# Optimization experiments

Hardware: AMD Instinct MI355X
Metric: run time of the kernel (lower is better)

Reference implementation:

```python
import jax, jax.numpy as jnp
import numpy as np

B, T, D, H, L, V, CTX = 4, 2048, 256, 8, 12, 256, 2048
HD = D // H


def _ln(x, w, b, eps=1e-5):
    m = x.mean(-1, keepdims=True)
    v = ((x - m) ** 2).mean(-1, keepdims=True)
    return (x - m) * jax.lax.rsqrt(v + eps) * w + b


def setup_inputs() -> dict:
    key = jax.random.key(0)
    ks = jax.random.split(key, 16)
    s = 0.02
    inp = {
        "x": jax.random.randint(ks[0], (B, T), 0, V, dtype=jnp.int32),
        "tok_embed": jax.random.normal(ks[1], (V, D), jnp.float32) * s,
        "pos_embed": jax.random.normal(ks[2], (CTX, D), jnp.float32) * s,
        # stacked per-layer params (leading axis = layer)
        "ln1_w": jnp.ones((L, D), jnp.float32),
        "ln1_b": jnp.zeros((L, D), jnp.float32),
        "qkv_w": jax.random.normal(ks[3], (L, D, 3 * D), jnp.float32) * s,
        "qkv_b": jnp.zeros((L, 3 * D), jnp.float32),
        "out_w": jax.random.normal(ks[4], (L, D, D), jnp.float32) * s,
        "out_b": jnp.zeros((L, D), jnp.float32),
        "ln2_w": jnp.ones((L, D), jnp.float32),
        "ln2_b": jnp.zeros((L, D), jnp.float32),
        "fc1_w": jax.random.normal(ks[5], (L, D, 4 * D), jnp.float32) * s,
        "fc1_b": jnp.zeros((L, 4 * D), jnp.float32),
        "fc2_w": jax.random.normal(ks[6], (L, 4 * D, D), jnp.float32) * s,
        "fc2_b": jnp.zeros((L, D), jnp.float32),
        "lnf_w": jnp.ones((D,), jnp.float32),
        "lnf_b": jnp.zeros((D,), jnp.float32),
        "head_w": jax.random.normal(ks[7], (D, V), jnp.float32) * s,
        "head_b": jnp.zeros((V,), jnp.float32),
    }
    return inp


def _forward(x, tok_embed, pos_embed, ln1_w, ln1_b, qkv_w, qkv_b, out_w, out_b,
             ln2_w, ln2_b, fc1_w, fc1_b, fc2_w, fc2_b, lnf_w, lnf_b, head_w, head_b):
    Tcur = x.shape[1]
    h = tok_embed[x] + pos_embed[:Tcur][None, :, :]  # (B,T,D)
    causal = jnp.triu(jnp.ones((Tcur, Tcur), bool), k=1)  # True above diagonal
    scale = jnp.sqrt(jnp.asarray(HD, h.dtype))

    def step(h, p):
        (l1w, l1b, qw, qb, ow, ob, l2w, l2b, f1w, f1b, f2w, f2b) = p
        # attention
        z = _ln(h, l1w, l1b)
        qkv = z @ qw + qb  # (B,T,3D)
        qkv = qkv.reshape(h.shape[0], Tcur, 3, H, HD)
        q, k, v = qkv[:, :, 0], qkv[:, :, 1], qkv[:, :, 2]  # (B,T,H,HD)
        attn = jnp.einsum('bqhd,bkhd->bhqk', q, k) / scale
        attn = jnp.where(causal, -jnp.inf, attn)
        attn = jax.nn.softmax(attn, axis=-1)
        o = jnp.einsum('bhqk,bkhd->bqhd', attn, v).reshape(h.shape[0], Tcur, D)
        h = h + o @ ow + ob
        # MLP (torch nn.GELU default = exact erf gelu)
        z = _ln(h, l2w, l2b)
        z = jax.nn.gelu(z @ f1w + f1b, approximate=False)
        h = h + z @ f2w + f2b
        return h, None

    params = (ln1_w, ln1_b, qkv_w, qkv_b, out_w, out_b,
              ln2_w, ln2_b, fc1_w, fc1_b, fc2_w, fc2_b)
    h, _ = jax.lax.scan(step, h, params)
    h = _ln(h, lnf_w, lnf_b)
    return h @ head_w + head_b  # (B,T,V)


def reference(x, tok_embed, pos_embed, ln1_w, ln1_b, qkv_w, qkv_b, out_w, out_b,
              ln2_w, ln2_b, fc1_w, fc1_b, fc2_w, fc2_b, lnf_w, lnf_b, head_w, head_b):
    return _forward(x, tok_embed, pos_embed, ln1_w, ln1_b, qkv_w, qkv_b, out_w, out_b,
                    ln2_w, ln2_b, fc1_w, fc1_b, fc2_w, fc2_b, lnf_w, lnf_b, head_w, head_b)
```

## Files before the change

### kernel.cpp

```cpp
#include <hip/hip_runtime.h>
#include <cstdint>

#define TT 2048
#define DD 256
#define HH 8
#define LL 12

typedef __attribute__((ext_vector_type(8))) short s16x8;
typedef __attribute__((ext_vector_type(4))) float f32x4;

__device__ __forceinline__ unsigned short f2bf(float f) {
  union { float f; unsigned u; } v; v.f = f;
  return (unsigned short)((v.u + 0x7FFFu + ((v.u >> 16) & 1u)) >> 16);
}

__device__ __forceinline__ float geluf(float x) {
  return 0.5f * x * (1.0f + erff(x * 0.70710678118654752f));
}

__device__ __forceinline__ float fexp2(float x) {
  float r;
  asm("v_exp_f32 %0, %1" : "=v"(r) : "v"(x));
  return r;
}

__device__ __forceinline__ void gload16(const void* g, void* l) {
  __builtin_amdgcn_global_load_lds((const __attribute__((address_space(1))) unsigned int*)g,
                                   (__attribute__((address_space(3))) unsigned int*)l, 16, 0, 0);
}

__global__ __launch_bounds__(256) void k_embed(const int* __restrict__ x,
                                               const float* __restrict__ tok,
                                               const float* __restrict__ pos,
                                               float* __restrict__ h) {
  int i = blockIdx.x * 256 + threadIdx.x;
  int row = i >> 6, c = i & 63;
  int t = x[row];
  f32x4 tv = ((const f32x4*)(tok + (size_t)t * DD))[c];
  f32x4 pv = ((const f32x4*)(pos + (size_t)(row & (TT - 1)) * DD))[c];
  ((f32x4*)(h + (size_t)row * DD))[c] = tv + pv;
}

__global__ __launch_bounds__(256) void k_ln(const float* __restrict__ h,
                                            const float* __restrict__ wgt,
                                            const float* __restrict__ bia,
                                            unsigned short* __restrict__ z) {
  int row = blockIdx.x * 4 + (threadIdx.x >> 6);
  int lane = threadIdx.x & 63;
  f32x4 v = ((const f32x4*)(h + (size_t)row * DD))[lane];
  float s = v[0] + v[1] + v[2] + v[3];
#pragma unroll
  for (int m = 32; m; m >>= 1) s += __shfl_xor(s, m);
  float mean = s * (1.0f / DD);
  f32x4 d = v - mean;
  float s2 = d[0] * d[0] + d[1] * d[1] + d[2] * d[2] + d[3] * d[3];
#pragma unroll
  for (int m = 32; m; m >>= 1) s2 += __shfl_xor(s2, m);
  float inv = rsqrtf(s2 * (1.0f / DD) + 1e-5f);
  f32x4 wv = ((const f32x4*)wgt)[lane];
  f32x4 bv = ((const f32x4*)bia)[lane];
  union { unsigned short us[4]; unsigned long long u64; } ou;
#pragma unroll
  for (int e = 0; e < 4; ++e) ou.us[e] = f2bf(d[e] * inv * wv[e] + bv[e]);
  *(unsigned long long*)(z + (size_t)row * DD + lane * 4) = ou.u64;
}

__global__ __launch_bounds__(256) void k_cast_all(const float* __restrict__ qw, const float* __restrict__ ow,
                                                  const float* __restrict__ f1, const float* __restrict__ f2,
                                                  unsigned short* __restrict__ dst) {
  const int l = blockIdx.y;
  const int t0 = blockIdx.x * 256 + threadIdx.x;
  const int stride = gridDim.x * 256;
  const float* qwl = qw + (size_t)l * 196608;
  const float* owl = ow + (size_t)l * 65536;
  const float* f1l = f1 + (size_t)l * 262144;
  const float* f2l = f2 + (size_t)l * 262144;
  unsigned short* dq = dst + (size_t)l * 786432;
  unsigned short* dO = dq + 196608;
  unsigned short* d1 = dO + 65536;
  unsigned short* d2 = d1 + 262144;
  for (int i = t0; i < 196608; i += stride) { int k = i / 768, n = i % 768; dq[n * 256 + k] = f2bf(qwl[i]); }
  for (int i = t0; i < 65536; i += stride) { int k = i >> 8, n = i & 255; dO[n * 256 + k] = f2bf(owl[i]); }
  for (int i = t0; i < 262144; i += stride) { int k = i >> 10, n = i & 1023; d1[n * 256 + k] = f2bf(f1l[i]); }
  for (int i = t0; i < 262144; i += stride) { int k = i >> 8, n = i & 255; d2[n * 1024 + k] = f2bf(f2l[i]); }
}

__global__ __launch_bounds__(256) void k_cast_tr4(const float* __restrict__ qw, const float* __restrict__ ow,
                                                  const float* __restrict__ f1, const float* __restrict__ f2,
                                                  unsigned short* __restrict__ dq, unsigned short* __restrict__ dO,
                                                  unsigned short* __restrict__ d1, unsigned short* __restrict__ d2) {
  int t0 = blockIdx.x * 256 + threadIdx.x;
  int stride = gridDim.x * 256;
  for (int i = t0; i < 256 * 768; i += stride) { int k = i / 768, n = i % 768; dq[n * 256 + k] = f2bf(qw[i]); }
  for (int i = t0; i < 256 * 256; i += stride) { int k = i >> 8, n = i & 255; dO[n * 256 + k] = f2bf(ow[i]); }
  for (int i = t0; i < 256 * 1024; i += stride) { int k = i >> 10, n = i & 1023; d1[n * 256 + k] = f2bf(f1[i]); }
  for (int i = t0; i < 1024 * 256; i += stride) { int k = i >> 8, n = i & 255; d2[n * 1024 + k] = f2bf(f2[i]); }
}

__global__ __launch_bounds__(256) void k_cast_tr256(const float* __restrict__ src, unsigned short* __restrict__ dst) {
  int i = blockIdx.x * 256 + threadIdx.x;
  int k = i >> 8, n = i & 255;
  dst[n * 256 + k] = f2bf(src[i]);
}

template <int MODE, int MI>
__global__ __launch_bounds__(256) void k_gemm(const unsigned short* __restrict__ A,
                                              const unsigned short* __restrict__ BT,
                                              const float* __restrict__ bias,
                                              void* out, const float* resid,
                                              int M, int N, int K) {
  __shared__ __align__(16) unsigned short As[MI * 32 * 64];
  __shared__ __align__(16) unsigned short Bs[128 * 64];
  const int tid = threadIdx.x;
  const int lane = tid & 63, wv = tid >> 6;
  const int wr = wv >> 1, wc = wv & 1;
  const int l15 = lane & 15, g = lane >> 4;
  const int BM = MI * 32;
  const int tm = blockIdx.y, tn = blockIdx.x;
  f32x4 acc[MI][4] = {};
  const int nk = K >> 6;
  const unsigned short* Ag0 = A + (size_t)tm * BM * K;
  const unsigned short* Bg0 = BT + (size_t)tn * 128 * K;
  for (int kt = 0; kt < nk; ++kt) {
#pragma unroll
    for (int it = 0; it < MI; ++it) {
      int chunk = it * 256 + tid;
      int row = chunk >> 3, part = chunk & 7;
      gload16(Ag0 + (size_t)row * K + kt * 64 + part * 8, As + chunk * 8);
    }
#pragma unroll
    for (int it = 0; it < 4; ++it) {
      int chunk = it * 256 + tid;
      int row = chunk >> 3, part = chunk & 7;
      gload16(Bg0 + (size_t)row * K + kt * 64 + part * 8, Bs + chunk * 8);
    }
    __syncthreads();
#pragma unroll
    for (int ks = 0; ks < 2; ++ks) {
      s16x8 af[MI], bf[4];
#pragma unroll
      for (int mi = 0; mi < MI; ++mi)
        af[mi] = *(const s16x8*)(As + (wr * MI * 16 + mi * 16 + l15) * 64 + ks * 32 + g * 8);
#pragma unroll
      for (int ni = 0; ni < 4; ++ni)
        bf[ni] = *(const s16x8*)(Bs + (wc * 64 + ni * 16 + l15) * 64 + ks * 32 + g * 8);
#pragma unroll
      for (int mi = 0; mi < MI; ++mi)
#pragma unroll
        for (int ni = 0; ni < 4; ++ni)
          acc[mi][ni] = __builtin_amdgcn_mfma_f32_16x16x32_bf16(af[mi], bf[ni], acc[mi][ni], 0, 0, 0);
    }
    __syncthreads();
  }
#pragma unroll
  for (int ni = 0; ni < 4; ++ni) {
    int col = tn * 128 + wc * 64 + ni * 16 + l15;
    float bv = bias[col];
#pragma unroll
    for (int mi = 0; mi < MI; ++mi) {
      int row0 = tm * BM + wr * MI * 16 + mi * 16 + g * 4;
#pragma unroll
      for (int r = 0; r < 4; ++r) {
        size_t idx = (size_t)(row0 + r) * N + col;
        float vvv = acc[mi][ni][r] + bv;
        if (MODE == 0) ((unsigned short*)out)[idx] = f2bf(vvv);
        else if (MODE == 1) ((unsigned short*)out)[idx] = f2bf(geluf(vvv));
        else if (MODE == 2) ((float*)out)[idx] = resid[idx] + vvv;
        else ((float*)out)[idx] = vvv;
      }
    }
  }
}

__global__ __launch_bounds__(256, 2) void k_attn(const unsigned short* __restrict__ qkv,
                                                 unsigned short* __restrict__ o) {
  __shared__ __align__(16) unsigned short Ks[2][128 * 40];
  __shared__ __align__(16) unsigned short Vs[2][2 * 32 * 72];
  __shared__ __align__(16) unsigned short Ps[4][2 * 16 * 72];
  const int tid = threadIdx.x, lane = tid & 63, w = tid >> 6;
  const int l15 = lane & 15, g = lane >> 4;
  const int p = blockIdx.x;
  const int b = blockIdx.y >> 3, hh = blockIdx.y & 7;
  const size_t base = (size_t)b * TT * 768 + hh * 32;
  const float scl2 = 0.25503492f;
  const int qt0 = p, qt1 = 31 - p;
  const int nt0 = (qt0 >> 1) + 1;
  const int kr = tid >> 1, khf = tid & 1;
  const int vk = tid & 127, vdh = tid >> 7;
  const int vkh = vk >> 6, vklo = vk & 63;
  unsigned short* Pw = &Ps[w][0];

  s16x8 qf0 = *(const s16x8*)(qkv + base + (size_t)(qt0 * 64 + w * 16 + l15) * 768 + g * 8);
  s16x8 qf1 = *(const s16x8*)(qkv + base + (size_t)(qt1 * 64 + w * 16 + l15) * 768 + g * 8);

  {
    const unsigned short* kp = qkv + base + (size_t)kr * 768 + 256 + khf * 16;
    s16x8 k0 = *(const s16x8*)kp;
    s16x8 k1 = *(const s16x8*)(kp + 8);
    const unsigned short* vp = qkv + base + (size_t)vk * 768 + 512 + vdh * 16;
    s16x8 v0 = *(const s16x8*)vp;
    s16x8 v1 = *(const s16x8*)(vp + 8);
    *(s16x8*)(Ks[0] + kr * 40 + khf * 16) = k0;
    *(s16x8*)(Ks[0] + kr * 40 + khf * 16 + 8) = k1;
    unsigned short* vb = Vs[0] + vkh * 2304;
#pragma unroll
    for (int e = 0; e < 8; ++e) {
      int d0 = vdh * 16 + e, d1 = vdh * 16 + 8 + e;
      vb[d0 * 72 + (vklo ^ (((d0 >> 3) & 3) << 4))] = (unsigned short)v0[e];
      vb[d1 * 72 + (vklo ^ (((d1 >> 3) & 3) << 4))] = (unsigned short)v1[e];
    }
  }
  __syncthreads();

  f32x4 accO[2] = {};
  float mM = -3.0e38f, ls = 0.f;

  for (int t = 0; t < 17; ++t) {
    const int buf = t & 1;
    const bool ph = (t >= nt0);
    const int qt = ph ? qt1 : qt0;
    const int j = ph ? t - nt0 : t;
    const bool have_next = (t + 1 < 17);
    s16x8 k0n, k1n, v0n, v1n;
    if (have_next) {
      const int jn = (t + 1 >= nt0) ? t + 1 - nt0 : t + 1;
      const unsigned short* kp = qkv + base + (size_t)(jn * 128 + kr) * 768 + 256 + khf * 16;
      k0n = *(const s16x8*)kp;
      k1n = *(const s16x8*)(kp + 8);
      const unsigned short* vp = qkv + base + (size_t)(jn * 128 + vk) * 768 + 512 + vdh * 16;
      v0n = *(const s16x8*)vp;
      v1n = *(const s16x8*)(vp + 8);
    }
    const int rel = qt * 64 + w * 16 - j * 128;
    const bool full = (rel >= 127);
    int cbm = (rel + 15) >> 4; if (cbm > 7) cbm = 7;
    f32x4 st[8];
#pragma unroll
    for (int cb = 0; cb < 8; ++cb)
      if (cb <= cbm) {
        s16x8 kf = *(const s16x8*)(Ks[buf] + (cb * 16 + l15) * 40 + g * 8);
        f32x4 zz = {};
        st[cb] = __builtin_amdgcn_mfma_f32_16x16x32_bf16(kf, ph ? qf1 : qf0, zz, 0, 0, 0);
      }
    float rmax = -3.0e38f;
#pragma unroll
    for (int cb = 0; cb < 8; ++cb)
      if (cb <= cbm) {
#pragma unroll
        for (int r = 0; r < 4; ++r) {
          float s = st[cb][r] * scl2;
          if (!full && (cb * 16 + g * 4 + r) > rel + l15) s = -3.0e38f;
          st[cb][r] = s;
          rmax = fmaxf(rmax, s);
        }
      }
    rmax = fmaxf(rmax, __shfl_xor(rmax, 16));
    rmax = fmaxf(rmax, __shfl_xor(rmax, 32));
    float al = 1.0f;
    if (!__all(rmax <= mM + 11.5f)) {
      float nm = fmaxf(mM, rmax);
      al = fexp2(mM - nm);
      mM = nm;
#pragma unroll
      for (int r = 0; r < 4; ++r) {
        float aw = __shfl(al, g * 4 + r);
        accO[0][r] *= aw;
        accO[1][r] *= aw;
      }
    }
    float rsum = 0.f;
#pragma unroll
    for (int cb = 0; cb < 8; ++cb)
      if (cb <= cbm) {
        union { unsigned short us[4]; unsigned long long u; } pk;
#pragma unroll
        for (int r = 0; r < 4; ++r) {
          float pe = fexp2(st[cb][r] - mM);
          rsum += pe;
          pk.us[r] = f2bf(pe);
        }
        *(unsigned long long*)(Pw + (cb >> 2) * 1152 + l15 * 72 + (cb & 3) * 16 + g * 4) = pk.u;
      }
    if (cbm < 7 && !(cbm & 1))
      *(unsigned long long*)(Pw + ((cbm + 1) >> 2) * 1152 + l15 * 72 + ((cbm + 1) & 3) * 16 + g * 4) = 0ULL;
    rsum += __shfl_xor(rsum, 16);
    rsum += __shfl_xor(rsum, 32);
    ls = ls * al + rsum;
    asm volatile("s_waitcnt lgkmcnt(0)" ::: "memory");
    __builtin_amdgcn_sched_barrier(0);
    const int kcm = cbm >> 1;
#pragma unroll
    for (int kc = 0; kc < 4; ++kc)
      if (kc <= kcm) {
        s16x8 pa = *(const s16x8*)(Pw + (kc >> 1) * 1152 + l15 * 72 + (kc & 1) * 32 + g * 8);
        s16x8 bv0, bv1;
#pragma unroll
        for (int hb = 0; hb < 2; ++hb) {
          const int d = hb * 16 + l15;
          const int kxr = ((kc & 1) * 32 + g * 8) ^ (((d >> 3) & 3) << 4);
          if (hb == 0) bv0 = *(const s16x8*)(Vs[buf] + (kc >> 1) * 2304 + d * 72 + kxr);
          else bv1 = *(const s16x8*)(Vs[buf] + (kc >> 1) * 2304 + d * 72 + kxr);
        }
        accO[0] = __builtin_amdgcn_mfma_f32_16x16x32_bf16(pa, bv0, accO[0], 0, 0, 0);
        accO[1] = __builtin_amdgcn_mfma_f32_16x16x32_bf16(pa, bv1, accO[1], 0, 0, 0);
      }
    if (have_next) {
      *(s16x8*)(Ks[buf ^ 1] + kr * 40 + khf * 16) = k0n;
      *(s16x8*)(Ks[buf ^ 1] + kr * 40 + khf * 16 + 8) = k1n;
      unsigned short* vb = Vs[buf ^ 1] + vkh * 2304;
#pragma unroll
      for (int e = 0; e < 8; ++e) {
        int d0 = vdh * 16 + e, d1 = vdh * 16 + 8 + e;
        vb[d0 * 72 + (vklo ^ (((d0 >> 3) & 3) << 4))] = (unsigned short)v0n[e];
        vb[d1 * 72 + (vklo ^ (((d1 >> 3) & 3) << 4))] = (unsigned short)v1n[e];
      }
      __syncthreads();
    }
    if (t == nt0 - 1) {
      float inv = 1.0f / ls;
#pragma unroll
      for (int r = 0; r < 4; ++r) {
        float lv = __shfl(inv, g * 4 + r);
        int row = qt0 * 64 + w * 16 + g * 4 + r;
        o[(size_t)(b * TT + row) * DD + hh * 32 + l15] = f2bf(accO[0][r] * lv);
        o[(size_t)(b * TT + row) * DD + hh * 32 + 16 + l15] = f2bf(accO[1][r] * lv);
      }
      accO[0] = f32x4{};
      accO[1] = f32x4{};
      mM = -3.0e38f;
      ls = 0.f;
    }
  }
  {
    float inv = 1.0f / ls;
#pragma unroll
    for (int r = 0; r < 4; ++r) {
      float lv = __shfl(inv, g * 4 + r);
      int row = qt1 * 64 + w * 16 + g * 4 + r;
      o[(size_t)(b * TT + row) * DD + hh * 32 + l15] = f2bf(accO[0][r] * lv);
      o[(size_t)(b * TT + row) * DD + hh * 32 + 16 + l15] = f2bf(accO[1][r] * lv);
    }
  }
}

extern "C" void kernel_launch(void* const* d_in, const int* in_sizes, int n_in,
                              void* d_out, int out_size, void* d_ws, size_t ws_size,
                              hipStream_t stream) {
  const int* x = (const int*)d_in[0];
  const float* tok = (const float*)d_in[1];
  const float* pos = (const float*)d_in[2];
  const float* ln1w = (const float*)d_in[3];
  const float* ln1b = (const float*)d_in[4];
  const float* qkvw = (const float*)d_in[5];
  const float* qkvb = (const float*)d_in[6];
  const float* outw = (const float*)d_in[7];
  const float* outb = (const float*)d_in[8];
  const float* ln2w = (const float*)d_in[9];
  const float* ln2b = (const float*)d_in[10];
  const float* f1w = (const float*)d_in[11];
  const float* f1b = (const float*)d_in[12];
  const float* f2w = (const float*)d_in[13];
  const float* f2b = (const float*)d_in[14];
  const float* lnfw = (const float*)d_in[15];
  const float* lnfb = (const float*)d_in[16];
  const float* hw = (const float*)d_in[17];
  const float* hb = (const float*)d_in[18];

  char* ws = (char*)d_ws;
  float* h = (float*)(ws + 0);
  unsigned short* z = (unsigned short*)(ws + 8388608);
  unsigned short* qkvB = (unsigned short*)(ws + 12582912);
  unsigned short* ob = (unsigned short*)(ws + 25165824);
  unsigned short* a1 = (unsigned short*)(ws + 29360128);
  unsigned short* wAll = (unsigned short*)(ws + 46137344);
  const bool bigws = ws_size >= 65142784ULL;
  unsigned short* wh = (unsigned short*)(ws + (bigws ? 65011712 : 47710208));

  if (bigws)
    k_cast_all<<<dim3(256, 12), dim3(256), 0, stream>>>(qkvw, outw, f1w, f2w, wAll);
  k_cast_tr256<<<dim3(256), dim3(256), 0, stream>>>(hw, wh);
  k_embed<<<dim3(2048), dim3(256), 0, stream>>>(x, tok, pos, h);

  for (int l = 0; l < LL; ++l) {
    unsigned short* wq = wAll + (size_t)(bigws ? l : 0) * 786432;
    unsigned short* wo = wq + 196608;
    unsigned short* w1 = wo + 65536;
    unsigned short* w2 = w1 + 262144;
    if (!bigws)
      k_cast_tr4<<<dim3(1024), dim3(256), 0, stream>>>(
          qkvw + (size_t)l * 196608, outw + (size_t)l * 65536,
          f1w + (size_t)l * 262144, f2w + (size_t)l * 262144, wq, wo, w1, w2);
    k_ln<<<dim3(2048), dim3(256), 0, stream>>>(h, ln1w + l * 256, ln1b + l * 256, z);
    k_gemm<0, 4><<<dim3(6, 64), dim3(256), 0, stream>>>(z, wq, qkvb + l * 768, qkvB, nullptr, 8192, 768, 256);
    k_attn<<<dim3(16, 32), dim3(256), 0, stream>>>(qkvB, ob);
    k_gemm<2, 2><<<dim3(2, 128), dim3(256), 0, stream>>>(ob, wo, outb + l * 256, h, h, 8192, 256, 256);
    k_ln<<<dim3(2048), dim3(256), 0, stream>>>(h, ln2w + l * 256, ln2b + l * 256, z);
    k_gemm<1, 4><<<dim3(8, 64), dim3(256), 0, stream>>>(z, w1, f1b + l * 1024, a1, nullptr, 8192, 1024, 256);
    k_gemm<2, 2><<<dim3(2, 128), dim3(256), 0, stream>>>(a1, w2, f2b + l * 256, h, h, 8192, 256, 1024);
  }

  k_ln<<<dim3(2048), dim3(256), 0, stream>>>(h, lnfw, lnfb, z);
  k_gemm<3, 2><<<dim3(2, 128), dim3(256), 0, stream>>>(z, wh, hb, d_out, nullptr, 8192, 256, 256);
}
```

Before: 1.544 ms.

## Double-buffer GEMM shared tiles and make weight-cast writes coalesced

The GEMM kernel now keeps two LDS buffers and issues the global loads for the next K tile before running the MFMAs on the current one, so memory latency can overlap with compute and one barrier per iteration goes away. Launch bounds now request two blocks per CU. The weight cast/transpose kernels are changed to write their output contiguously and gather strided reads instead. Double buffering doubles LDS use per block, which can lower occupancy, and the gload16 helper (not shown) may be synchronous, in which case little overlap is gained.

Result: no change. 1.551 ms (+0.5%).

```diff
diff --git a/kernel.cpp b/kernel.cpp
--- a/kernel.cpp
+++ b/kernel.cpp
@@ -79,10 +79,10 @@
   unsigned short* dO = dq + 196608;
   unsigned short* d1 = dO + 65536;
   unsigned short* d2 = d1 + 262144;
-  for (int i = t0; i < 196608; i += stride) { int k = i / 768, n = i % 768; dq[n * 256 + k] = f2bf(qwl[i]); }
-  for (int i = t0; i < 65536; i += stride) { int k = i >> 8, n = i & 255; dO[n * 256 + k] = f2bf(owl[i]); }
-  for (int i = t0; i < 262144; i += stride) { int k = i >> 10, n = i & 1023; d1[n * 256 + k] = f2bf(f1l[i]); }
-  for (int i = t0; i < 262144; i += stride) { int k = i >> 8, n = i & 255; d2[n * 1024 + k] = f2bf(f2l[i]); }
+  for (int i = t0; i < 196608; i += stride) dq[i] = f2bf(qwl[(i & 255) * 768 + (i >> 8)]);
+  for (int i = t0; i < 65536; i += stride) dO[i] = f2bf(owl[(i & 255) * 256 + (i >> 8)]);
+  for (int i = t0; i < 262144; i += stride) d1[i] = f2bf(f1l[(i & 255) * 1024 + (i >> 8)]);
+  for (int i = t0; i < 262144; i += stride) d2[i] = f2bf(f2l[(i & 1023) * 256 + (i >> 10)]);
 }
 
 __global__ __launch_bounds__(256) void k_cast_tr4(const float* __restrict__ qw, const float* __restrict__ ow,
@@ -91,26 +91,25 @@
                                                   unsigned short* __restrict__ d1, unsigned short* __restrict__ d2) {
   int t0 = blockIdx.x * 256 + threadIdx.x;
   int stride = gridDim.x * 256;
-  for (int i = t0; i < 256 * 768; i += stride) { int k = i / 768, n = i % 768; dq[n * 256 + k] = f2bf(qw[i]); }
-  for (int i = t0; i < 256 * 256; i += stride) { int k = i >> 8, n = i & 255; dO[n * 256 + k] = f2bf(ow[i]); }
-  for (int i = t0; i < 256 * 1024; i += stride) { int k = i >> 10, n = i & 1023; d1[n * 256 + k] = f2bf(f1[i]); }
-  for (int i = t0; i < 1024 * 256; i += stride) { int k = i >> 8, n = i & 255; d2[n * 1024 + k] = f2bf(f2[i]); }
+  for (int i = t0; i < 196608; i += stride) dq[i] = f2bf(qw[(i & 255) * 768 + (i >> 8)]);
+  for (int i = t0; i < 65536; i += stride) dO[i] = f2bf(ow[(i & 255) * 256 + (i >> 8)]);
+  for (int i = t0; i < 262144; i += stride) d1[i] = f2bf(f1[(i & 255) * 1024 + (i >> 8)]);
+  for (int i = t0; i < 262144; i += stride) d2[i] = f2bf(f2[(i & 1023) * 256 + (i >> 10)]);
 }
 
 __global__ __launch_bounds__(256) void k_cast_tr256(const float* __restrict__ src, unsigned short* __restrict__ dst) {
   int i = blockIdx.x * 256 + threadIdx.x;
-  int k = i >> 8, n = i & 255;
-  dst[n * 256 + k] = f2bf(src[i]);
+  dst[i] = f2bf(src[(i & 255) * 256 + (i >> 8)]);
 }
 
 template <int MODE, int MI>
-__global__ __launch_bounds__(256) void k_gemm(const unsigned short* __restrict__ A,
-                                              const unsigned short* __restrict__ BT,
-                                              const float* __restrict__ bias,
-                                              void* out, const float* resid,
-                                              int M, int N, int K) {
-  __shared__ __align__(16) unsigned short As[MI * 32 * 64];
-  __shared__ __align__(16) unsigned short Bs[128 * 64];
+__global__ __launch_bounds__(256, 2) void k_gemm(const unsigned short* __restrict__ A,
+                                                 const unsigned short* __restrict__ BT,
+                                                 const float* __restrict__ bias,
+                                                 void* out, const float* resid,
+                                                 int M, int N, int K) {
+  __shared__ __align__(16) unsigned short As[2][MI * 32 * 64];
+  __shared__ __align__(16) unsigned short Bs[2][128 * 64];
   const int tid = threadIdx.x;
   const int lane = tid & 63, wv = tid >> 6;
   const int wr = wv >> 1, wc = wv & 1;
@@ -121,36 +120,48 @@
   const int nk = K >> 6;
   const unsigned short* Ag0 = A + (size_t)tm * BM * K;
   const unsigned short* Bg0 = BT + (size_t)tn * 128 * K;
+  const int srow = tid >> 3, spart = tid & 7;
+
+#pragma unroll
+  for (int it = 0; it < MI; ++it)
+    gload16(Ag0 + (size_t)(it * 32 + srow) * K + spart * 8, As[0] + (it * 256 + tid) * 8);
+#pragma unroll
+  for (int it = 0; it < 4; ++it)
+    gload16(Bg0 + (size_t)(it * 32 + srow) * K + spart * 8, Bs[0] + (it * 256 + tid) * 8);
+  __syncthreads();
+
+  int buf = 0;
   for (int kt = 0; kt < nk; ++kt) {
-#pragma unroll
-    for (int it = 0; it < MI; ++it) {
-      int chunk = it * 256 + tid;
-      int row = chunk >> 3, part = chunk & 7;
-      gload16(Ag0 + (size_t)row * K + kt * 64 + part * 8, As + chunk * 8);
-    }
-#pragma unroll
-    for (int it = 0; it < 4; ++it) {
-      int chunk = it * 256 + tid;
-      int row = chunk >> 3, part = chunk & 7;
-      gload16(Bg0 + (size_t)row * K + kt * 64 + part * 8, Bs + chunk * 8);
-    }
-    __syncthreads();
+    const bool have_next = (kt + 1 < nk);
+    if (have_next) {
+#pragma unroll
+      for (int it = 0; it < MI; ++it)
+        gload16(Ag0 + (size_t)(it * 32 + srow) * K + (kt + 1) * 64 + spart * 8,
+                As[buf ^ 1] + (it * 256 + tid) * 8);
+#pragma unroll
+      for (int it = 0; it < 4; ++it)
+        gload16(Bg0 + (size_t)(it * 32 + srow) * K + (kt + 1) * 64 + spart * 8,
+                Bs[buf ^ 1] + (it * 256 + tid) * 8);
+    }
 #pragma unroll
     for (int ks = 0; ks < 2; ++ks) {
       s16x8 af[MI], bf[4];
 #pragma unroll
       for (int mi = 0; mi < MI; ++mi)
-        af[mi] = *(const s16x8*)(As + (wr * MI * 16 + mi * 16 + l15) * 64 + ks * 32 + g * 8);
+        af[mi] = *(const s16x8*)(As[buf] + (wr * MI * 16 + mi * 16 + l15) * 64 + ks * 32 + g * 8);
 #pragma unroll
       for (int ni = 0; ni < 4; ++ni)
-        bf[ni] = *(const s16x8*)(Bs + (wc * 64 + ni * 16 + l15) * 64 + ks * 32 + g * 8);
+        bf[ni] = *(const s16x8*)(Bs[buf] + (wc * 64 + ni * 16 + l15) * 64 + ks * 32 + g * 8);
 #pragma unroll
       for (int mi = 0; mi < MI; ++mi)
 #pragma unroll
         for (int ni = 0; ni < 4; ++ni)
           acc[mi][ni] = __builtin_amdgcn_mfma_f32_16x16x32_bf16(af[mi], bf[ni], acc[mi][ni], 0, 0, 0);
     }
-    __syncthreads();
+    if (have_next) {
+      __syncthreads();
+      buf ^= 1;
+    }
   }
 #pragma unroll
   for (int ni = 0; ni < 4; ++ni) {
```
